# Performance work log

Measured on AMD Instinct MI355X. Metric: run time of the kernel, lower is better.

## Reference

```python
import jax, jax.numpy as jnp
import numpy as np
import math

H = 64   # hidden_size
N = 512  # num_objects
B = 128  # batch


def setup_inputs() -> dict:
    key = jax.random.key(0)
    ks = jax.random.split(key, 10)
    q = jax.random.normal(ks[0], (N, B, H), dtype=jnp.float32)
    k = jax.random.normal(ks[1], (N, B, H), dtype=jnp.float32)
    v = jax.random.normal(ks[2], (N, B, H), dtype=jnp.float32)
    # binary visibility mask [B, N, N]
    batch_traffic_id_map = (jax.random.uniform(ks[3], (B, N, N)) < 0.7).astype(jnp.float32)
    s = 1.0 / math.sqrt(H)
    Wq = jax.random.uniform(ks[4], (H, H), minval=-s, maxval=s, dtype=jnp.float32)
    bq = jax.random.uniform(ks[5], (H,), minval=-s, maxval=s, dtype=jnp.float32)
    Wk = jax.random.uniform(ks[6], (H, H), minval=-s, maxval=s, dtype=jnp.float32)
    bk = jax.random.uniform(ks[7], (H,), minval=-s, maxval=s, dtype=jnp.float32)
    Wv = jax.random.uniform(ks[8], (H, H), minval=-s, maxval=s, dtype=jnp.float32)
    bv = jax.random.uniform(ks[9], (H,), minval=-s, maxval=s, dtype=jnp.float32)
    return {"q": q, "k": k, "v": v, "batch_traffic_id_map": batch_traffic_id_map,
            "Wq": Wq, "bq": bq, "Wk": Wk, "bk": bk, "Wv": Wv, "bv": bv}


def reference(q, k, v, batch_traffic_id_map, Wq, bq, Wk, bk, Wv, bv):
    hidden_size = q.shape[-1]
    # Linear projections then transpose(0,1): [N,B,H] -> [B,N,H]
    qp = jnp.einsum('nbh,kh->bnk', q, Wq) + bq
    kp = jnp.einsum('nbh,kh->bnk', k, Wk) + bk
    vp = jnp.einsum('nbh,kh->bnk', v, Wv) + bv
    # scaled scores, exp, mask, custom sum-normalization
    a = jnp.einsum('bnh,bmh->bnm', qp, kp) / jnp.sqrt(jnp.float32(hidden_size))
    a = jnp.exp(a) * batch_traffic_id_map
    a_sum = jnp.sum(a, axis=-1)                      # [B, N]
    a_sum = jnp.where(a_sum == 0, jnp.ones_like(a_sum), a_sum)
    A = a / a_sum[..., None]                          # [B, N, N]
    out = jnp.einsum('bnm,bmh->nbh', A, vp)           # matmul + transpose(0,1)
    # dropout is identity in eval mode
    return out, A
```

## Files before the change

kernel.cpp:

```cpp
#include <hip/hip_runtime.h>

#define H 64
#define NOBJ 512
#define BATCH 128

typedef __attribute__((ext_vector_type(8))) short s16x8;
typedef __attribute__((ext_vector_type(4))) float f32x4;
typedef __attribute__((ext_vector_type(4))) unsigned short u16x4;
typedef __attribute__((ext_vector_type(8))) unsigned short u16x8;

__device__ __forceinline__ unsigned short f2bf(float f) {
    unsigned int u = __float_as_uint(f);
    u += 0x7FFFu + ((u >> 16) & 1u);
    return (unsigned short)(u >> 16);
}
__device__ __forceinline__ float bf2f(unsigned short h) {
    return __uint_as_float((unsigned int)h << 16);
}

#define MFMA16(a, b, c) __builtin_amdgcn_mfma_f32_16x16x32_bf16(a, b, c, 0, 0, 0)

__global__ __launch_bounds__(256) void proj_kernel(
    const float* __restrict__ q, const float* __restrict__ k, const float* __restrict__ v,
    const float* __restrict__ Wq, const float* __restrict__ bq,
    const float* __restrict__ Wk, const float* __restrict__ bk,
    const float* __restrict__ Wv, const float* __restrict__ bv,
    unsigned short* __restrict__ qh, unsigned short* __restrict__ ql,
    unsigned short* __restrict__ kh, unsigned short* __restrict__ kl,
    unsigned short* __restrict__ vt)
{
    __shared__ unsigned short vtile[64][72];

    const int z = blockIdx.z;
    const float* x; const float* W; const float* bias;
    unsigned short* yh; unsigned short* yl;
    if (z == 0)      { x = q; W = Wq; bias = bq; yh = qh; yl = ql; }
    else if (z == 1) { x = k; W = Wk; bias = bk; yh = kh; yl = kl; }
    else             { x = v; W = Wv; bias = bv; yh = nullptr; yl = nullptr; }

    const int tid  = threadIdx.x;
    const int lane = tid & 63;
    const int wt   = tid >> 6;
    const int l15  = lane & 15;
    const int lg   = lane >> 4;
    const int n0   = blockIdx.x * 64;
    const int b    = blockIdx.y;

    s16x8 wfh[4][2], wfl[4][2];
    #pragma unroll
    for (int ht = 0; ht < 4; ++ht) {
        #pragma unroll
        for (int kc = 0; kc < 2; ++kc) {
            const float* p = W + (ht * 16 + l15) * H + kc * 32 + lg * 8;
            float4 f0 = *(const float4*)p;
            float4 f1 = *(const float4*)(p + 4);
            float f[8] = {f0.x, f0.y, f0.z, f0.w, f1.x, f1.y, f1.z, f1.w};
            s16x8 hi8, lo8;
            #pragma unroll
            for (int j = 0; j < 8; ++j) {
                const unsigned short hb = f2bf(f[j]);
                hi8[j] = (short)hb;
                lo8[j] = (short)f2bf(f[j] - bf2f(hb));
            }
            wfh[ht][kc] = hi8; wfl[ht][kc] = lo8;
        }
    }

    const int n = n0 + wt * 16 + l15;
    const float* xr = x + ((size_t)n * BATCH + b) * H;
    s16x8 xfh[2], xfl[2];
    #pragma unroll
    for (int kc = 0; kc < 2; ++kc) {
        const float* p = xr + kc * 32 + lg * 8;
        float4 f0 = *(const float4*)p;
        float4 f1 = *(const float4*)(p + 4);
        float f[8] = {f0.x, f0.y, f0.z, f0.w, f1.x, f1.y, f1.z, f1.w};
        s16x8 hi8, lo8;
        #pragma unroll
        for (int j = 0; j < 8; ++j) {
            const unsigned short hb = f2bf(f[j]);
            hi8[j] = (short)hb;
            lo8[j] = (short)f2bf(f[j] - bf2f(hb));
        }
        xfh[kc] = hi8; xfl[kc] = lo8;
    }

    if (z < 2) {
        #pragma unroll
        for (int ht = 0; ht < 4; ++ht) {
            const float4 b4 = *(const float4*)(bias + ht * 16 + lg * 4);
            f32x4 acc = {b4.x, b4.y, b4.z, b4.w};
            acc = MFMA16(wfh[ht][0], xfh[0], acc);
            acc = MFMA16(wfh[ht][1], xfh[1], acc);
            acc = MFMA16(wfh[ht][0], xfl[0], acc);
            acc = MFMA16(wfh[ht][1], xfl[1], acc);
            acc = MFMA16(wfl[ht][0], xfh[0], acc);
            acc = MFMA16(wfl[ht][1], xfh[1], acc);
            u16x4 hv, lv;
            #pragma unroll
            for (int r = 0; r < 4; ++r) {
                const unsigned short hb = f2bf(acc[r]);
                hv[r] = hb;
                lv[r] = f2bf(acc[r] - bf2f(hb));
            }
            const size_t o = ((size_t)b * NOBJ + n) * H + ht * 16 + lg * 4;
            *(u16x4*)(yh + o) = hv;
            *(u16x4*)(yl + o) = lv;
        }
    } else {
        #pragma unroll
        for (int ht = 0; ht < 4; ++ht) {
            const float bs = bias[ht * 16 + l15];
            f32x4 acc = {bs, bs, bs, bs};
            acc = MFMA16(xfh[0], wfh[ht][0], acc);
            acc = MFMA16(xfh[1], wfh[ht][1], acc);
            acc = MFMA16(xfl[0], wfh[ht][0], acc);
            acc = MFMA16(xfl[1], wfh[ht][1], acc);
            acc = MFMA16(xfh[0], wfl[ht][0], acc);
            acc = MFMA16(xfh[1], wfl[ht][1], acc);
            u16x4 hv;
            #pragma unroll
            for (int r = 0; r < 4; ++r) hv[r] = f2bf(acc[r]);
            *(u16x4*)&vtile[ht * 16 + l15][wt * 16 + lg * 4] = hv;
        }
        __syncthreads();
        const int h = tid >> 2, nc = (tid & 3) * 16;
        const u16x8 d0 = *(const u16x8*)&vtile[h][nc];
        const u16x8 d1 = *(const u16x8*)&vtile[h][nc + 8];
        unsigned short* dst = vt + ((size_t)b * H + h) * NOBJ + n0 + nc;
        *(u16x8*)dst = d0;
        *(u16x8*)(dst + 8) = d1;
    }
}

__global__ __launch_bounds__(256, 4) void attn_kernel(
    const unsigned short* __restrict__ qh, const unsigned short* __restrict__ ql,
    const unsigned short* __restrict__ kh, const unsigned short* __restrict__ kl,
    const unsigned short* __restrict__ vt, const float* __restrict__ mask,
    float* __restrict__ out, float* __restrict__ Aout)
{
    __shared__ unsigned short sch[16][520];
    __shared__ unsigned short scl[16][520];
    __shared__ float rsum[4][16];
    __shared__ float inv[16];

    const int tid  = threadIdx.x;
    const int lane = tid & 63;
    const int w    = tid >> 6;
    const int l15  = lane & 15;
    const int lg   = lane >> 4;
    const int n0   = blockIdx.x * 16;
    const int b    = blockIdx.y;

    const size_t qoff = ((size_t)b * NOBJ + n0 + l15) * H + lg * 8;
    const s16x8 qfh0 = *(const s16x8*)(qh + qoff);
    const s16x8 qfh1 = *(const s16x8*)(qh + qoff + 32);
    const s16x8 qfl0 = *(const s16x8*)(ql + qoff);
    const s16x8 qfl1 = *(const s16x8*)(ql + qoff + 32);

    const unsigned short* khp = kh + ((size_t)b * NOBJ + w * 128 + l15) * H + lg * 8;
    const unsigned short* klp = kl + ((size_t)b * NOBJ + w * 128 + l15) * H + lg * 8;
    const float* mskp = mask + ((size_t)b * NOBJ + n0 + l15) * NOBJ + w * 128 + lg * 4;

    f32x4 ev[8];
    float rp = 0.0f;

    #pragma unroll
    for (int mt = 0; mt < 8; ++mt) {
        const s16x8 kf_h0 = *(const s16x8*)(khp + (mt * 16) * H);
        const s16x8 kf_h1 = *(const s16x8*)(khp + (mt * 16) * H + 32);
        const s16x8 kf_l0 = *(const s16x8*)(klp + (mt * 16) * H);
        const s16x8 kf_l1 = *(const s16x8*)(klp + (mt * 16) * H + 32);
        const float4 msk  = *(const float4*)(mskp + mt * 16);

        f32x4 acc = {0.0f, 0.0f, 0.0f, 0.0f};
        acc = MFMA16(kf_h0, qfh0, acc);
        acc = MFMA16(kf_h1, qfh1, acc);
        acc = MFMA16(kf_h0, qfl0, acc);
        acc = MFMA16(kf_h1, qfl1, acc);
        acc = MFMA16(kf_l0, qfh0, acc);
        acc = MFMA16(kf_l1, qfh1, acc);

        f32x4 e;
        e[0] = __expf(acc[0] * 0.125f) * msk.x;
        e[1] = __expf(acc[1] * 0.125f) * msk.y;
        e[2] = __expf(acc[2] * 0.125f) * msk.z;
        e[3] = __expf(acc[3] * 0.125f) * msk.w;
        ev[mt] = e;
        rp += (e[0] + e[1]) + (e[2] + e[3]);

        u16x4 hv, lv;
        #pragma unroll
        for (int r = 0; r < 4; ++r) {
            const unsigned short hb = f2bf(e[r]);
            hv[r] = hb;
            lv[r] = f2bf(e[r] - bf2f(hb));
        }
        const int mo = w * 128 + mt * 16 + lg * 4;
        *(u16x4*)&sch[l15][mo] = hv;
        *(u16x4*)&scl[l15][mo] = lv;
    }

    rp += __shfl_xor(rp, 16);
    rp += __shfl_xor(rp, 32);
    if (lane < 16) rsum[w][lane] = rp;
    __syncthreads();
    if (tid < 16) {
        const float s = (rsum[0][tid] + rsum[1][tid]) + (rsum[2][tid] + rsum[3][tid]);
        inv[tid] = 1.0f / (s == 0.0f ? 1.0f : s);
    }
    __syncthreads();

    {
        const float iv = inv[l15];
        float* Arow = Aout + ((size_t)b * NOBJ + n0 + l15) * NOBJ + w * 128 + lg * 4;
        #pragma unroll
        for (int mt = 0; mt < 8; ++mt) {
            float4 a4;
            a4.x = ev[mt][0] * iv; a4.y = ev[mt][1] * iv;
            a4.z = ev[mt][2] * iv; a4.w = ev[mt][3] * iv;
            *(float4*)(Arow + mt * 16) = a4;
        }
    }

    const unsigned short* vtp = vt + ((size_t)b * H + w * 16 + l15) * NOBJ + lg * 8;
    f32x4 o0 = {0.0f, 0.0f, 0.0f, 0.0f}, o1 = {0.0f, 0.0f, 0.0f, 0.0f};
    #pragma unroll
    for (int ks = 0; ks < 16; ks += 2) {
        const int mk = ks * 32 + lg * 8;
        const s16x8 ah0 = *(const s16x8*)&sch[l15][mk];
        const s16x8 al0 = *(const s16x8*)&scl[l15][mk];
        const s16x8 vf0 = *(const s16x8*)(vtp + ks * 32);
        o0 = MFMA16(ah0, vf0, o0);
        o0 = MFMA16(al0, vf0, o0);
        const s16x8 ah1 = *(const s16x8*)&sch[l15][mk + 32];
        const s16x8 al1 = *(const s16x8*)&scl[l15][mk + 32];
        const s16x8 vf1 = *(const s16x8*)(vtp + ks * 32 + 32);
        o1 = MFMA16(ah1, vf1, o1);
        o1 = MFMA16(al1, vf1, o1);
    }

    #pragma unroll
    for (int r = 0; r < 4; ++r) {
        const int nn = lg * 4 + r;
        out[((size_t)(n0 + nn) * BATCH + b) * H + w * 16 + l15] = (o0[r] + o1[r]) * inv[nn];
    }
}

extern "C" void kernel_launch(void* const* d_in, const int* in_sizes, int n_in,
                              void* d_out, int out_size, void* d_ws, size_t ws_size,
                              hipStream_t stream)
{
    (void)in_sizes; (void)n_in; (void)out_size; (void)ws_size;
    const float* q    = (const float*)d_in[0];
    const float* k    = (const float*)d_in[1];
    const float* v    = (const float*)d_in[2];
    const float* mask = (const float*)d_in[3];
    const float* Wq   = (const float*)d_in[4];
    const float* bq   = (const float*)d_in[5];
    const float* Wk   = (const float*)d_in[6];
    const float* bk   = (const float*)d_in[7];
    const float* Wv   = (const float*)d_in[8];
    const float* bv   = (const float*)d_in[9];

    float* out  = (float*)d_out;
    float* Aout = (float*)d_out + (size_t)NOBJ * BATCH * H;

    const size_t S = (size_t)BATCH * NOBJ * H;
    unsigned short* qh = (unsigned short*)d_ws;
    unsigned short* ql = qh + S;
    unsigned short* kh = ql + S;
    unsigned short* kl = kh + S;
    unsigned short* vt = kl + S;

    proj_kernel<<<dim3(NOBJ / 64, BATCH, 3), 256, 0, stream>>>(
        q, k, v, Wq, bq, Wk, bk, Wv, bv, qh, ql, kh, kl, vt);
    attn_kernel<<<dim3(NOBJ / 16, BATCH), 256, 0, stream>>>(
        qh, ql, kh, kl, vt, mask, out, Aout);
}
```

Measured before the change: 401.5 us.

## Pack visibility mask into bitfields and double-buffer K fragment loads

Adds a pre-pass kernel that reads the float mask with fully coalesced loads and compresses it into one bit per entry. The attention kernel then reads one uint4 of bits per row instead of scattered float4 mask loads. It also prefetches the next K tile's fragments while the MFMAs run on the current one. The full float mask is still read once, so total traffic is about the same and there is an extra launch plus a bitfield write. The bit form treats any nonzero mask value as 1, which is only exact for a binary mask.

```diff
diff --git a/kernel.cpp b/kernel.cpp
--- a/kernel.cpp
+++ b/kernel.cpp
@@ -19,6 +19,27 @@
 }
 
 #define MFMA16(a, b, c) __builtin_amdgcn_mfma_f32_16x16x32_bf16(a, b, c, 0, 0, 0)
+
+__global__ __launch_bounds__(256) void mask_pack_kernel(
+    const float* __restrict__ mask, unsigned int* __restrict__ bits)
+{
+    __shared__ unsigned char nib[256];
+    const int tid = threadIdx.x;
+    const size_t base = (size_t)blockIdx.x * 1024;
+    const float4 f = *(const float4*)(mask + base + (size_t)tid * 4);
+    nib[tid] = (unsigned char)((unsigned)(f.x != 0.0f)
+             | ((unsigned)(f.y != 0.0f) << 1)
+             | ((unsigned)(f.z != 0.0f) << 2)
+             | ((unsigned)(f.w != 0.0f) << 3));
+    __syncthreads();
+    if (tid < 32) {
+        unsigned int wv = 0;
+        #pragma unroll
+        for (int i = 0; i < 8; ++i)
+            wv |= (unsigned int)nib[tid * 8 + i] << (4 * i);
+        bits[base / 32 + tid] = wv;
+    }
+}
 
 __global__ __launch_bounds__(256) void proj_kernel(
     const float* __restrict__ q, const float* __restrict__ k, const float* __restrict__ v,
@@ -136,7 +157,7 @@
 __global__ __launch_bounds__(256, 4) void attn_kernel(
     const unsigned short* __restrict__ qh, const unsigned short* __restrict__ ql,
     const unsigned short* __restrict__ kh, const unsigned short* __restrict__ kl,
-    const unsigned short* __restrict__ vt, const float* __restrict__ mask,
+    const unsigned short* __restrict__ vt, const unsigned int* __restrict__ bits,
     float* __restrict__ out, float* __restrict__ Aout)
 {
     __shared__ unsigned short sch[16][520];
@@ -160,32 +181,45 @@
 
     const unsigned short* khp = kh + ((size_t)b * NOBJ + w * 128 + l15) * H + lg * 8;
     const unsigned short* klp = kl + ((size_t)b * NOBJ + w * 128 + l15) * H + lg * 8;
-    const float* mskp = mask + ((size_t)b * NOBJ + n0 + l15) * NOBJ + w * 128 + lg * 4;
+
+    const uint4 mw = *(const uint4*)(bits + ((size_t)b * NOBJ + n0 + l15) * (NOBJ / 32) + w * 4);
+    const unsigned mwa[4] = {mw.x, mw.y, mw.z, mw.w};
 
     f32x4 ev[8];
     float rp = 0.0f;
 
+    s16x8 ka[2][4];
+    ka[0][0] = *(const s16x8*)(khp);
+    ka[0][1] = *(const s16x8*)(khp + 32);
+    ka[0][2] = *(const s16x8*)(klp);
+    ka[0][3] = *(const s16x8*)(klp + 32);
+
     #pragma unroll
     for (int mt = 0; mt < 8; ++mt) {
-        const s16x8 kf_h0 = *(const s16x8*)(khp + (mt * 16) * H);
-        const s16x8 kf_h1 = *(const s16x8*)(khp + (mt * 16) * H + 32);
-        const s16x8 kf_l0 = *(const s16x8*)(klp + (mt * 16) * H);
-        const s16x8 kf_l1 = *(const s16x8*)(klp + (mt * 16) * H + 32);
-        const float4 msk  = *(const float4*)(mskp + mt * 16);
+        const int cur = mt & 1, nxt = cur ^ 1;
+        if (mt < 7) {
+            const int o = (mt + 1) * 16 * H;
+            ka[nxt][0] = *(const s16x8*)(khp + o);
+            ka[nxt][1] = *(const s16x8*)(khp + o + 32);
+            ka[nxt][2] = *(const s16x8*)(klp + o);
+            ka[nxt][3] = *(const s16x8*)(klp + o + 32);
+        }
 
         f32x4 acc = {0.0f, 0.0f, 0.0f, 0.0f};
-        acc = MFMA16(kf_h0, qfh0, acc);
-        acc = MFMA16(kf_h1, qfh1, acc);
-        acc = MFMA16(kf_h0, qfl0, acc);
-        acc = MFMA16(kf_h1, qfl1, acc);
-        acc = MFMA16(kf_l0, qfh0, acc);
-        acc = MFMA16(kf_l1, qfh1, acc);
-
+        acc = MFMA16(ka[cur][0], qfh0, acc);
+        acc = MFMA16(ka[cur][1], qfh1, acc);
+        acc = MFMA16(ka[cur][0], qfl0, acc);
+        acc = MFMA16(ka[cur][1], qfl1, acc);
+        acc = MFMA16(ka[cur][2], qfh0, acc);
+        acc = MFMA16(ka[cur][3], qfh1, acc);
+
+        const unsigned wsel = mwa[mt >> 1] >> (((mt & 1) << 4) + (lg << 2));
         f32x4 e;
-        e[0] = __expf(acc[0] * 0.125f) * msk.x;
-        e[1] = __expf(acc[1] * 0.125f) * msk.y;
-        e[2] = __expf(acc[2] * 0.125f) * msk.z;
-        e[3] = __expf(acc[3] * 0.125f) * msk.w;
+        #pragma unroll
+        for (int r = 0; r < 4; ++r) {
+            const float ex = __expf(acc[r] * 0.125f);
+            e[r] = ((wsel >> r) & 1u) ? ex : 0.0f;
+        }
         ev[mt] = e;
         rp += (e[0] + e[1]) + (e[2] + e[3]);
 
@@ -272,9 +306,11 @@
     unsigned short* kh = ql + S;
     unsigned short* kl = kh + S;
     unsigned short* vt = kl + S;
-
+    unsigned int* bits = (unsigned int*)(vt + S);
+
+    mask_pack_kernel<<<dim3((BATCH * NOBJ * NOBJ) / 1024), 256, 0, stream>>>(mask, bits);
     proj_kernel<<<dim3(NOBJ / 64, BATCH, 3), 256, 0, stream>>>(
         q, k, v, Wq, bq, Wk, bk, Wv, bv, qh, ql, kh, kl, vt);
     attn_kernel<<<dim3(NOBJ / 16, BATCH), 256, 0, stream>>>(
-        qh, ql, kh, kl, vt, mask, out, Aout);
-}
+        qh, ql, kh, kl, vt, bits, out, Aout);
+}
```

Result: no change. 398.1 us (-0.8%).
